# Performance work log

Hardware: AMD Instinct MI355X
Metric: run time of the kernel (lower is better)

Reference implementation:

```python
import jax, jax.numpy as jnp
import numpy as np

B, SEQ, D, H, L, DFF, K = 2, 2048, 256, 8, 2, 1024, 3
DK = D // H
EPS = 1e-5
DROP_CONNECT = 0.5  # eval mode: weight * (1 - rate)


def _make_pe():
    pos = np.arange(SEQ)[:, None].astype(np.float32)
    div = np.exp(np.arange(0, D, 2).astype(np.float32) * (-np.log(10000.0) / D))
    pe = np.zeros((SEQ, D), np.float32)
    pe[:, 0::2] = np.sin(pos * div)
    pe[:, 1::2] = np.cos(pos * div)
    return jnp.asarray(pe)


def setup_inputs() -> dict:
    key = jax.random.key(0)
    ks = jax.random.split(key, 16)
    s = 0.02
    d = {
        'x': jax.random.normal(ks[0], (B, SEQ, 1), jnp.float32),
        'conv_w': jax.random.normal(ks[1], (D, 1, K), jnp.float32) * s,
        'conv_b': jnp.zeros((D,), jnp.float32),
        'bn_g': jnp.ones((D,), jnp.float32),
        'bn_b': jnp.zeros((D,), jnp.float32),
        'pe': _make_pe(),
        'qW': jax.random.normal(ks[2], (L, D, D), jnp.float32) * s,
        'qb': jnp.zeros((L, D), jnp.float32),
        'kW': jax.random.normal(ks[3], (L, D, D), jnp.float32) * s,
        'kb': jnp.zeros((L, D), jnp.float32),
        'vW': jax.random.normal(ks[4], (L, D, D), jnp.float32) * s,
        'vb': jnp.zeros((L, D), jnp.float32),
        'oW': jax.random.normal(ks[5], (L, D, D), jnp.float32) * s,
        'ob': jnp.zeros((L, D), jnp.float32),
        'scale': jnp.ones((L,), jnp.float32),
        'td': jnp.ones((L, H), jnp.float32),
        'ln1g': jnp.ones((L, D), jnp.float32),
        'ln1b': jnp.zeros((L, D), jnp.float32),
        'f1W': jax.random.normal(ks[6], (L, DFF, D), jnp.float32) * s,
        'f1b': jnp.zeros((L, DFF), jnp.float32),
        'f2W': jax.random.normal(ks[7], (L, D, DFF), jnp.float32) * s,
        'f2b': jnp.zeros((L, D), jnp.float32),
        'ln2g': jnp.ones((L, D), jnp.float32),
        'ln2b': jnp.zeros((L, D), jnp.float32),
        'outW': jax.random.normal(ks[8], (1, D), jnp.float32) * s,
        'outb': jnp.zeros((1,), jnp.float32),
    }
    return d


def _layernorm(z, g, b):
    m = z.mean(-1, keepdims=True)
    v = ((z - m) ** 2).mean(-1, keepdims=True)
    return (z - m) / jnp.sqrt(v + EPS) * g + b


def reference(x, conv_w, conv_b, bn_g, bn_b, pe, qW, qb, kW, kb, vW, vb, oW, ob,
              scale, td, ln1g, ln1b, f1W, f1b, f2W, f2b, ln2g, ln2b, outW, outb):
    # CNN frontend: [B,S,1] -> [B,1,S] -> conv -> BN(eval) -> relu -> [B,S,D]
    h = jnp.transpose(x, (0, 2, 1))
    h = jax.lax.conv_general_dilated(h, conv_w, (1,), 'SAME',
                                     dimension_numbers=('NCH', 'OIH', 'NCH'))
    h = h + conv_b[None, :, None]
    # BatchNorm eval with running_mean=0, running_var=1
    h = h / jnp.sqrt(1.0 + EPS) * bn_g[None, :, None] + bn_b[None, :, None]
    h = jax.nn.relu(h)
    h = jnp.transpose(h, (0, 2, 1)) + pe[None]

    inv_sqrt_dk = 1.0 / np.sqrt(DK).astype(np.float32)
    key_pos = jnp.arange(SEQ, dtype=h.dtype)  # decay depends on key index only

    for l in range(L):
        q = (h @ qW[l].T + qb[l]).reshape(B, SEQ, H, DK).transpose(0, 2, 1, 3)
        k = (h @ kW[l].T + kb[l]).reshape(B, SEQ, H, DK).transpose(0, 2, 1, 3)
        v = (h @ vW[l].T + vb[l]).reshape(B, SEQ, H, DK).transpose(0, 2, 1, 3)
        scores = jnp.einsum('bhqd,bhkd->bhqk', q, k) * (inv_sqrt_dk * scale[l])
        decay = jnp.exp(-td[l][:, None, None] * key_pos[None, None, :])  # [H,1,S]
        scores = scores * decay[None]
        attn = jax.nn.softmax(scores, axis=-1) * jax.nn.sigmoid(scores)
        ctx = jnp.einsum('bhqk,bhkd->bhqd', attn, v)
        ctx = ctx.transpose(0, 2, 1, 3).reshape(B, SEQ, D)
        h = _layernorm(h + (ctx @ oW[l].T + ob[l]), ln1g[l], ln1b[l])
        ff = jax.nn.relu(h @ f1W[l].T + f1b[l]) @ f2W[l].T + f2b[l]
        h = _layernorm(h + ff, ln2g[l], ln2b[l])

    last = h[:, -1, :]
    # DropConnectLinear in eval: weight * (1 - drop_connect_rate)
    return last @ (outW * (1.0 - DROP_CONNECT)).T + outb
```

## Files before the change

### kernel.cpp

```cpp
#include <hip/hip_runtime.h>
#include <math.h>

#define B_    2
#define SEQ_  2048
#define D_    256
#define H_    8
#define DK_   32
#define L_    2
#define DFF_  1024

#define TD_CUT 44.0f

typedef short  bf16x8 __attribute__((ext_vector_type(8)));
typedef float  f32x4  __attribute__((ext_vector_type(4)));

__device__ __forceinline__ int compute_kcut(float tdv) {
    int kcut = SEQ_;
    if (tdv > 1e-9f) {
        float kc = TD_CUT / tdv;
        kcut = (kc >= (float)SEQ_) ? SEQ_ : ((int)kc + 1);
    }
    int kcr = (kcut + 63) & ~63;
    if (kcr > SEQ_) kcr = SEQ_;
    return kcr;
}

__device__ __forceinline__ unsigned short f2bf(float f) {
    unsigned int u = __float_as_uint(f);
    unsigned int r = u + 0x7FFFu + ((u >> 16) & 1u);
    return (unsigned short)(r >> 16);
}
__device__ __forceinline__ float bf2f(unsigned short u) {
    return __uint_as_float(((unsigned int)u) << 16);
}
__device__ __forceinline__ float bflo(unsigned int u) {
    return __uint_as_float(u << 16);
}
__device__ __forceinline__ float bfhi(unsigned int u) {
    return __uint_as_float(u & 0xFFFF0000u);
}

__device__ __forceinline__ void gload_lds16(const unsigned short* g, unsigned short* l) {
    __builtin_amdgcn_global_load_lds(
        (const __attribute__((address_space(1))) unsigned int*)(const unsigned int*)g,
        (__attribute__((address_space(3))) unsigned int*)(unsigned int*)l,
        16, 0, 0);
}

__global__ __launch_bounds__(256) void prep_kernel(
    const float* __restrict__ x, const float* __restrict__ w,
    const float* __restrict__ cb, const float* __restrict__ bg,
    const float* __restrict__ bb, const float* __restrict__ pe,
    float* __restrict__ h, unsigned short* __restrict__ hbf,
    const float* __restrict__ p0, const float* __restrict__ p1,
    const float* __restrict__ p2, const float* __restrict__ p3,
    const float* __restrict__ p4, const float* __restrict__ p5,
    unsigned short* __restrict__ q0, unsigned short* __restrict__ q1,
    unsigned short* __restrict__ q2, unsigned short* __restrict__ q3,
    unsigned short* __restrict__ q4, unsigned short* __restrict__ q5,
    float* __restrict__ hts0, float* __restrict__ hts1)
{
    int bid = blockIdx.x;
// ... 36 lines not shown

    int s0 = tile * 32;
    float xm1 = (s0 > 0) ? xp[s0 - 1] : 0.f;
    float x0v = xp[s0];
    float hsum = 0.f;
#pragma unroll 4
    for (int r = 0; r < 32; ++r) {
        int s = s0 + r;
        float xp1 = (s < SEQ_ - 1) ? xp[s + 1] : 0.f;
        float acc = xm1 * w0 + x0v * w1v + xp1 * w2v + cbd;
        acc = acc * gg + bbd;
        acc = fmaxf(acc, 0.f);
        float v = acc + pe[s * D_ + d];
        size_t idx = ((size_t)(b * SEQ_ + s)) * D_ + d;
        h[idx] = v;
        unsigned short ub = f2bf(v);
        hbf[idx] = ub;
        hsum += bf2f(ub);
        xm1 = x0v; x0v = xp1;
    }
    hts0[(b * 64 + tile) * 256 + d] = hsum;
}

__global__ __launch_bounds__(256) void gemm_qkv(
    const unsigned short* __restrict__ A,
    const unsigned short* __restrict__ W0, const unsigned short* __restrict__ W1,
    const unsigned short* __restrict__ W2,
    const float* __restrict__ b0, const float* __restrict__ b1,
    const float* __restrict__ b2,
    unsigned short* __restrict__ O0, unsigned short* __restrict__ O1,
    unsigned short* __restrict__ O2,
    const float* __restrict__ td_l,
    const float* __restrict__ hts_l, float* __restrict__ vts_g,
    int M, int N, int K)
{
    __shared__ unsigned short As[2][2][2048];
    __shared__ unsigned short Bs[2][2][2048];
    __shared__ float hsc[256];

    int z = blockIdx.z;
    int tid  = threadIdx.x;

    if (z == 3) {
        if (blockIdx.x != 0 || blockIdx.y >= 16) return;
        int hh = blockIdx.y & 7;
        int b  = blockIdx.y >> 3;
        int kcr = compute_kcut(td_l[hh]);
        if (kcr >= SEQ_) return;
        int tcut = kcr >> 5;
        const float* hb = hts_l + (size_t)b * 64 * 256 + tid;
        float s = 0.f;
#pragma unroll
        for (int t = 0; t < 64; ++t) {
            float v = hb[t * 256];
            s += (t >= tcut) ? v : 0.f;
        }
        hsc[tid] = s;
        __syncthreads();
        int j = tid >> 3, e = tid & 7;
        const unsigned short* wrow = W2 + (size_t)(hh * 32 + j) * 256 + e * 32;
        float dot = 0.f;
#pragma unroll
        for (int i = 0; i < 4; ++i) {
            bf16x8 w8 = *(const bf16x8*)(wrow + i * 8);
#pragma unroll
            for (int t2 = 0; t2 < 8; ++t2)
                dot += hsc[e * 32 + i * 8 + t2] * bf2f((unsigned short)w8[t2]);
        }
        dot += __shfl_xor(dot, 1);
        dot += __shfl_xor(dot, 2);
        dot += __shfl_xor(dot, 4);
        if (e == 0)
            vts_g[(b * H_ + hh) * 32 + j] = dot + (float)(SEQ_ - kcr) * b2[hh * 32 + j];
        return;
    }

    int bm = blockIdx.y * 64, bn = blockIdx.x * 64;
    if (z > 0) {
        float tdmin = td_l[0];
#pragma unroll
        for (int i = 1; i < H_; ++i) tdmin = fminf(tdmin, td_l[i]);
        if ((bm & (SEQ_ - 1)) >= compute_kcut(tdmin)) return;
    }
    const unsigned short* W = (z == 0) ? W0 : (z == 1) ? W1 : W2;
    const float* bias = (z == 0) ? b0 : (z == 1) ? b1 : b2;
    unsigned short* C = (z == 0) ? O0 : (z == 1) ? O1 : O2;

    int wave = tid >> 6, lane = tid & 63;
    int wm = (wave & 1) * 32, wn = (wave >> 1) * 32;

    int sr  = tid >> 2;
    int scb = (tid & 3) ^ ((sr >> 1) & 3);
    const unsigned short* aG = A + (size_t)(bm + sr) * K + scb * 8;
    const unsigned short* wG = W + (size_t)(bn + sr) * K + scb * 8;

    int fr = lane & 15;
    int kb = lane >> 4;
    int cbo = (kb ^ ((fr >> 1) & 3)) * 8;
    int oA0 = (wm + fr) * 32 + cbo;
    int oA1 = (wm + 16 + fr) * 32 + cbo;
    int oB0 = (wn + fr) * 32 + cbo;
    int oB1 = (wn + 16 + fr) * 32 + cbo;

    f32x4 acc[2][2];
#pragma unroll
    for (int i = 0; i < 2; ++i)
#pragma unroll
        for (int j = 0; j < 2; ++j) acc[i][j] = (f32x4){0.f, 0.f, 0.f, 0.f};

    auto stage = [&](int s, int dd) {
        gload_lds16(aG + s * 64,      &As[dd][0][tid * 8]);
        gload_lds16(aG + s * 64 + 32, &As[dd][1][tid * 8]);
        gload_lds16(wG + s * 64,      &Bs[dd][0][tid * 8]);
        gload_lds16(wG + s * 64 + 32, &Bs[dd][1][tid * 8]);
    };

    int nst = K >> 6;
    stage(0, 0);
    __syncthreads();
    for (int s = 0; s < nst; ++s) {
        int dd = s & 1;
        if (s + 1 < nst) stage(s + 1, dd ^ 1);
#pragma unroll
        for (int kk = 0; kk < 2; ++kk) {
            bf16x8 a0f = *(const bf16x8*)&As[dd][kk][oA0];
            bf16x8 a1f = *(const bf16x8*)&As[dd][kk][oA1];
            bf16x8 b0f = *(const bf16x8*)&Bs[dd][kk][oB0];
            bf16x8 b1f = *(const bf16x8*)&Bs[dd][kk][oB1];
            acc[0][0] = __builtin_amdgcn_mfma_f32_16x16x32_bf16(a0f, b0f, acc[0][0], 0, 0, 0);
            acc[0][1] = __builtin_amdgcn_mfma_f32_16x16x32_bf16(a0f, b1f, acc[0][1], 0, 0, 0);
            acc[1][0] = __builtin_amdgcn_mfma_f32_16x16x32_bf16(a1f, b0f, acc[1][0], 0, 0, 0);
            acc[1][1] = __builtin_amdgcn_mfma_f32_16x16x32_bf16(a1f, b1f, acc[1][1], 0, 0, 0);
        }
        __syncthreads();
    }

    int crow = (lane >> 4) * 4;
    int ccol = lane & 15;
#pragma unroll
    for (int j = 0; j < 2; ++j) {
        float bj = bias[bn + wn + j * 16 + ccol];
#pragma unroll
        for (int i = 0; i < 2; ++i) {
#pragma unroll
            for (int r = 0; r < 4; ++r) {
                float v = acc[i][j][r] + bj;
                C[(size_t)(bm + wm + i * 16 + crow + r) * N + bn + wn + j * 16 + ccol] = f2bf(v);
            }
        }
    }
}

__global__ __launch_bounds__(256) void attn_kernel(
    const unsigned short* __restrict__ q, const unsigned short* __restrict__ k,
    const unsigned short* __restrict__ v, const float* __restrict__ vts_g,
    unsigned short* __restrict__ ctxbf,
    const float* __restrict__ scale_p, const float* __restrict__ td_l)
{
    int b = blockIdx.z, hh = blockIdx.y;
    int tid = threadIdx.x;
    int wave = tid >> 6, lane = tid & 63;
    int q0r = blockIdx.x * 64;

    float sc  = 0.17677669529663687f * scale_p[0];
    float tdv = td_l[hh];
    int kcr = compute_kcut(tdv);
    int ntiles = kcr >> 6;

    __shared__ unsigned short qt[64 * 32];
    __shared__ unsigned short kt[64 * 32];
    __shared__ unsigned short vtT[32 * 72];
    __shared__ unsigned short pl[64 * 72];
    __shared__ float vts_s[32];

    if (tid < 32) vts_s[tid] = vts_g[(b * H_ + hh) * 32 + tid];

    int srow = tid >> 2, sseg = tid & 3;
    gload_lds16(q + ((size_t)(b * SEQ_ + q0r + srow)) * D_ + hh * DK_ + sseg * 8,
                &qt[tid * 8]);

    int fr = lane & 15, kb = lane >> 4;
    const unsigned short* qfrag = &qt[(wave * 16 + fr) * 32 + kb * 8];

    f32x4 acc_o[2];
    acc_o[0] = (f32x4){0.f, 0.f, 0.f, 0.f};
    acc_o[1] = (f32x4){0.f, 0.f, 0.f, 0.f};
    float lpart[4] = {0.f, 0.f, 0.f, 0.f};

    for (int t = 0; t < ntiles; ++t) {
        int k0 = t * 64;
        if (t > 0) __syncthreads();
        {
            gload_lds16(k + ((size_t)(b * SEQ_ + k0 + srow)) * D_ + hh * DK_ + sseg * 8,
                        &kt[tid * 8]);
            const unsigned short* vp =
                v + ((size_t)(b * SEQ_ + k0 + srow)) * D_ + hh * DK_ + sseg * 8;
            uint4 uv = *(const uint4*)vp;
            unsigned short ve[8];
            ve[0] = (unsigned short)(uv.x); ve[1] = (unsigned short)(uv.x >> 16);
            ve[2] = (unsigned short)(uv.y); ve[3] = (unsigned short)(uv.y >> 16);
            ve[4] = (unsigned short)(uv.z); ve[5] = (unsigned short)(uv.z >> 16);
            ve[6] = (unsigned short)(uv.w); ve[7] = (unsigned short)(uv.w >> 16);
#pragma unroll
            for (int e = 0; e < 8; ++e)
                vtT[(sseg * 8 + e) * 72 + srow] = ve[e];
        }
        __syncthreads();

        f32x4 acc_s[4];
        bf16x8 aq = *(const bf16x8*)qfrag;
#pragma unroll
        for (int kt_i = 0; kt_i < 4; ++kt_i) {
            bf16x8 bk = *(const bf16x8*)&kt[(kt_i * 16 + fr) * 32 + kb * 8];
            acc_s[kt_i] = __builtin_amdgcn_mfma_f32_16x16x32_bf16(
                aq, bk, (f32x4){0.f, 0.f, 0.f, 0.f}, 0, 0, 0);
        }
#pragma unroll
        for (int kt_i = 0; kt_i < 4; ++kt_i) {
#pragma unroll
            for (int r = 0; r < 4; ++r) {
                int key = k0 + kt_i * 16 + fr;
                float sv = acc_s[kt_i][r] * sc * __expf(-tdv * (float)key);
                float e  = __expf(sv);
                float sg = 1.f / (1.f + __expf(-sv));
                lpart[r] += e;
                int qrow = wave * 16 + kb * 4 + r;
                pl[qrow * 72 + kt_i * 16 + fr] = f2bf(e * sg);
            }
        }
        __syncthreads();

#pragma unroll
        for (int ks = 0; ks < 2; ++ks) {
            bf16x8 pa = *(const bf16x8*)&pl[(wave * 16 + fr) * 72 + ks * 32 + kb * 8];
#pragma unroll
            for (int nt = 0; nt < 2; ++nt) {
                bf16x8 vb8 = *(const bf16x8*)&vtT[(nt * 16 + fr) * 72 + ks * 32 + kb * 8];
                acc_o[nt] = __builtin_amdgcn_mfma_f32_16x16x32_bf16(pa, vb8, acc_o[nt], 0, 0, 0);
            }
        }
    }

#pragma unroll
    for (int r = 0; r < 4; ++r) {
        lpart[r] += __shfl_xor(lpart[r], 1);
        lpart[r] += __shfl_xor(lpart[r], 2);
        lpart[r] += __shfl_xor(lpart[r], 4);
        lpart[r] += __shfl_xor(lpart[r], 8);
    }
    float taill = (kcr < SEQ_) ? (float)(SEQ_ - kcr) : 0.f;

#pragma unroll
    for (int nt = 0; nt < 2; ++nt) {
        float vadd = (kcr < SEQ_) ? 0.5f * vts_s[nt * 16 + fr] : 0.f;
#pragma unroll
        for (int r = 0; r < 4; ++r) {
            float invL = 1.f / (lpart[r] + taill);
            float o = (acc_o[nt][r] + vadd) * invL;
            int qrow = q0r + wave * 16 + kb * 4 + r;
            ctxbf[((size_t)(b * SEQ_ + qrow)) * D_ + hh * DK_ + nt * 16 + fr] = f2bf(o);
        }
    }
}

__global__ __launch_bounds__(256) void oproj_ln1(
    const unsigned short* __restrict__ ctx, const unsigned short* __restrict__ wo,
    const float* __restrict__ ob, const float* __restrict__ resid,
    const float* __restrict__ g1, const float* __restrict__ bt1,
    float* __restrict__ h1out, unsigned short* __restrict__ h1bf)
{
    __shared__ unsigned short As[2][512];
    __shared__ unsigned short Bs[2][8192];
    __shared__ float lsum[4][16], lsq[4][16], mean_s[16], inv_s[16];

    int tid = threadIdx.x;
    int wave = tid >> 6, lane = tid & 63;
    int bm = blockIdx.x * 16;
    int fr = lane & 15, kb = lane >> 4;
    int q = kb, cl = fr;
    int swz = (fr >> 1) & 3;

    const unsigned short* gpB[4];
    int dstB[4];
// ... 77 lines not shown
        float sq = lsq[0][tid] + lsq[1][tid] + lsq[2][tid] + lsq[3][tid];
        float mean = s * (1.f / 256.f);
        float var  = sq * (1.f / 256.f) - mean * mean;
        mean_s[tid] = mean;
        inv_s[tid]  = rsqrtf(var + 1e-5f);
    }
    __syncthreads();

#pragma unroll
    for (int ct = 0; ct < 4; ++ct) {
        int col = wave * 64 + ct * 16 + cl;
        float gc = g1[col], bc = bt1[col];
#pragma unroll
        for (int r = 0; r < 4; ++r) {
            int lr = q * 4 + r;
            float o = (zv[ct][r] - mean_s[lr]) * inv_s[lr] * gc + bc;
            size_t off = (size_t)(bm + lr) * 256 + col;
            h1out[off] = o;
            h1bf[off]  = f2bf(o);
        }
    }
}

__global__ __launch_bounds__(256) void ffn_fused(
    const unsigned short* __restrict__ h1bf, const unsigned short* __restrict__ w1,
    const float* __restrict__ f1b, const unsigned short* __restrict__ w2,
    float* __restrict__ part)
{
    __shared__ unsigned short As[2][1024];
    __shared__ unsigned short Bs[2][8192];
    __shared__ unsigned short ffs[32 * 264];

    int tid = threadIdx.x;
    int wave = tid >> 6, lane = tid & 63;
    int c = blockIdx.x;
    int bm = blockIdx.y * 32;
    int fr = lane & 15, kb = lane >> 4;
    int q = kb, cl = fr;

    const unsigned short* gB1[4];
    const unsigned short* gB2[4];
    int dstB[4];
#pragma unroll
    for (int i = 0; i < 4; ++i) {
        int sB = i * 256 + tid;
        int r = sB >> 2, ck = (sB & 3) ^ ((r >> 1) & 3);
        gB1[i] = w1 + (size_t)(c * 256 + r) * 256 + ck * 8;
        gB2[i] = w2 + (size_t)r * 1024 + c * 256 + ck * 8;
        dstB[i] = sB * 8;
    }
    const unsigned short* gA = nullptr;
    if (tid < 128) {
        int ar = tid >> 2, ack = (tid & 3) ^ ((ar >> 1) & 3);
        gA = h1bf + (size_t)(bm + ar) * 256 + ack * 8;
    }

    int oA1[2], oB[4];
#pragma unroll
    for (int t = 0; t < 2; ++t) {
        int m = t * 16 + fr;
        oA1[t] = m * 32 + ((kb ^ ((m >> 1) & 3)) * 8);
    }
#pragma unroll
    for (int t = 0; t < 4; ++t) {
        int n = wave * 64 + t * 16 + fr;
        oB[t] = n * 32 + ((kb ^ ((n >> 1) & 3)) * 8);
    }

    auto stage1 = [&](int s, int dd) {
#pragma unroll
        for (int i = 0; i < 4; ++i) gload_lds16(gB1[i] + s * 32, &Bs[dd][dstB[i]]);
        if (tid < 128) gload_lds16(gA + s * 32, &As[dd][tid * 8]);
    };
    auto stage2 = [&](int s, int dd) {
#pragma unroll
        for (int i = 0; i < 4; ++i) gload_lds16(gB2[i] + s * 32, &Bs[dd][dstB[i]]);
    };

    f32x4 a1[2][4];
#pragma unroll
    for (int i = 0; i < 2; ++i)
#pragma unroll
        for (int j = 0; j < 4; ++j) a1[i][j] = (f32x4){0.f, 0.f, 0.f, 0.f};

    stage1(0, 0);
    __syncthreads();
    for (int ks = 0; ks < 8; ++ks) {
        int dd = ks & 1;
        if (ks + 1 < 8) stage1(ks + 1, dd ^ 1);
        bf16x8 af[2], bfv[4];
#pragma unroll
        for (int t = 0; t < 2; ++t) af[t] = *(const bf16x8*)&As[dd][oA1[t]];
#pragma unroll
        for (int t = 0; t < 4; ++t) bfv[t] = *(const bf16x8*)&Bs[dd][oB[t]];
#pragma unroll
        for (int i = 0; i < 2; ++i)
#pragma unroll
            for (int j = 0; j < 4; ++j)
                a1[i][j] = __builtin_amdgcn_mfma_f32_16x16x32_bf16(af[i], bfv[j], a1[i][j], 0, 0, 0);
        __syncthreads();
    }

#pragma unroll
    for (int ct = 0; ct < 4; ++ct) {
        int col = wave * 64 + ct * 16 + cl;
        float bj = f1b[c * 256 + col];
#pragma unroll
        for (int rt = 0; rt < 2; ++rt)
#pragma unroll
            for (int r = 0; r < 4; ++r) {
                float v = fmaxf(a1[rt][ct][r] + bj, 0.f);
                ffs[(rt * 16 + q * 4 + r) * 264 + col] = f2bf(v);
            }
    }

    f32x4 a2[2][4];
#pragma unroll
    for (int i = 0; i < 2; ++i)
#pragma unroll
        for (int j = 0; j < 4; ++j) a2[i][j] = (f32x4){0.f, 0.f, 0.f, 0.f};

    stage2(0, 0);
    __syncthreads();
    for (int ks = 0; ks < 8; ++ks) {
        int dd = ks & 1;
        if (ks + 1 < 8) stage2(ks + 1, dd ^ 1);
        bf16x8 af[2], bfv[4];
#pragma unroll
        for (int t = 0; t < 2; ++t)
            af[t] = *(const bf16x8*)&ffs[(t * 16 + fr) * 264 + ks * 32 + kb * 8];
#pragma unroll
        for (int t = 0; t < 4; ++t) bfv[t] = *(const bf16x8*)&Bs[dd][oB[t]];
#pragma unroll
        for (int i = 0; i < 2; ++i)
#pragma unroll
            for (int j = 0; j < 4; ++j)
                a2[i][j] = __builtin_amdgcn_mfma_f32_16x16x32_bf16(af[i], bfv[j], a2[i][j], 0, 0, 0);
        __syncthreads();
    }

#pragma unroll
    for (int ct = 0; ct < 4; ++ct) {
        int col = wave * 64 + ct * 16 + cl;
#pragma unroll
        for (int rt = 0; rt < 2; ++rt)
#pragma unroll
            for (int r = 0; r < 4; ++r)
                part[((size_t)c * 4096 + bm + rt * 16 + q * 4 + r) * 256 + col] = a2[rt][ct][r];
    }
}

__global__ __launch_bounds__(256) void merge_ln2(
    const float* __restrict__ h1, const float* __restrict__ part,
    const float* __restrict__ f2b, const float* __restrict__ g2,
    const float* __restrict__ bt2,
    float* __restrict__ hout, unsigned short* __restrict__ hbf,
    const float* __restrict__ outW, const float* __restrict__ outb,
    float* __restrict__ out, int doFinal,
    float* __restrict__ hts1, int doHts)
{
    __shared__ float red[4][256];

    int wrp = threadIdx.x >> 6;
    int row = blockIdx.x * 4 + wrp;
    int lane = threadIdx.x & 63;
    int d = lane * 4;

    float4 z = *(const float4*)(h1 + (size_t)row * 256 + d);
    float4 b4 = *(const float4*)(f2b + d);
    z.x += b4.x; z.y += b4.y; z.z += b4.z; z.w += b4.w;
#pragma unroll
    for (int c = 0; c < 4; ++c) {
        float4 p = *(const float4*)(part + ((size_t)c * 4096 + row) * 256 + d);
        z.x += p.x; z.y += p.y; z.z += p.z; z.w += p.w;
    }

    float s = z.x + z.y + z.z + z.w;
    float ss = z.x * z.x + z.y * z.y + z.z * z.z + z.w * z.w;
#pragma unroll
    for (int off = 1; off < 64; off <<= 1) {
        s += __shfl_xor(s, off);
        ss += __shfl_xor(ss, off);
    }
    float mean = s * (1.f / 256.f);
    float var = ss * (1.f / 256.f) - mean * mean;
    float inv = rsqrtf(var + 1e-5f);

    float4 g4 = *(const float4*)(g2 + d);
    float4 t4 = *(const float4*)(bt2 + d);
    float4 o;
    o.x = (z.x - mean) * inv * g4.x + t4.x;
    o.y = (z.y - mean) * inv * g4.y + t4.y;
    o.z = (z.z - mean) * inv * g4.z + t4.z;
    o.w = (z.w - mean) * inv * g4.w + t4.w;
    *(float4*)(hout + (size_t)row * 256 + d) = o;
    unsigned short s0 = f2bf(o.x), s1 = f2bf(o.y), s2 = f2bf(o.z), s3 = f2bf(o.w);
    unsigned int u01 = (unsigned)s0 | ((unsigned)s1 << 16);
    unsigned int u23 = (unsigned)s2 | ((unsigned)s3 << 16);
    *(uint2*)&hbf[(size_t)row * 256 + d] = make_uint2(u01, u23);

    if (doHts) {
        *(float4*)&red[wrp][d] = make_float4(bf2f(s0), bf2f(s1), bf2f(s2), bf2f(s3));
        __syncthreads();
        int cidx = threadIdx.x;
        float cs = red[0][cidx] + red[1][cidx] + red[2][cidx] + red[3][cidx];
        int b = blockIdx.x >> 9;
        int tile = (blockIdx.x >> 3) & 63;
        atomicAdd(&hts1[((b << 6) + tile) * 256 + cidx], cs);
    }

    if (doFinal && (row == 2047 || row == 4095)) {
        float4 w4 = *(const float4*)(outW + d);
        float s2f = o.x * w4.x + o.y * w4.y + o.z * w4.z + o.w * w4.w;
#pragma unroll
        for (int off = 1; off < 64; off <<= 1) s2f += __shfl_xor(s2f, off);
        if (lane == 0) out[row >> 11] = s2f * 0.5f + outb[0];
    }
}

extern "C" void kernel_launch(void* const* d_in, const int* in_sizes, int n_in,
                              void* d_out, int out_size, void* d_ws, size_t ws_size,
                              hipStream_t stream)
{
    (void)in_sizes; (void)n_in; (void)out_size; (void)ws_size;
    const float* x      = (const float*)d_in[0];
    const float* conv_w = (const float*)d_in[1];
    const float* conv_b = (const float*)d_in[2];
    const float* bn_g   = (const float*)d_in[3];
    const float* bn_b   = (const float*)d_in[4];
    const float* pe     = (const float*)d_in[5];
    const float* qW     = (const float*)d_in[6];
    const float* qb     = (const float*)d_in[7];
    const float* kW     = (const float*)d_in[8];
    const float* kb     = (const float*)d_in[9];
    const float* vW     = (const float*)d_in[10];
    const float* vb     = (const float*)d_in[11];
    const float* oW     = (const float*)d_in[12];
    const float* ob     = (const float*)d_in[13];
    const float* scale  = (const float*)d_in[14];
// ... 2 lines not shown
    const float* ln1b   = (const float*)d_in[17];
    const float* f1W    = (const float*)d_in[18];
    const float* f1b    = (const float*)d_in[19];
    const float* f2W    = (const float*)d_in[20];
    const float* f2b    = (const float*)d_in[21];
    const float* ln2g   = (const float*)d_in[22];
    const float* ln2b   = (const float*)d_in[23];
    const float* outW   = (const float*)d_in[24];
    const float* outb   = (const float*)d_in[25];
    float* out = (float*)d_out;

    float* ws = (float*)d_ws;
    const size_t MT = (size_t)B_ * SEQ_ * D_;
    const size_t HTS = (size_t)B_ * 64 * 256;
    float* h     = ws;
    float* h1    = ws + MT;
    float* part  = ws + 2 * MT;
    float* hts0  = ws + 6 * MT;
    float* hts1  = hts0 + HTS;
    float* vts_g = hts1 + HTS;
    unsigned short* bfb = (unsigned short*)(vts_g + 512);
    unsigned short* h_bf   = bfb;
    unsigned short* ctx_bf = bfb + MT;
    unsigned short* q_bf   = bfb + 2 * MT;
    unsigned short* k_bf   = bfb + 3 * MT;
    unsigned short* v_bf   = bfb + 4 * MT;
    unsigned short* h1_bf  = bfb + 5 * MT;
    unsigned short* wq_bf  = bfb + 6 * MT;
    unsigned short* wk_bf  = wq_bf + MT / 8;
    unsigned short* wv_bf  = wk_bf + MT / 8;
    unsigned short* wo_bf  = wv_bf + MT / 8;
    unsigned short* wf1_bf = wo_bf + MT / 8;
    unsigned short* wf2_bf = wf1_bf + MT / 2;

    const int Mrows = B_ * SEQ_;

    prep_kernel<<<768 + 128, 256, 0, stream>>>(
        x, conv_w, conv_b, bn_g, bn_b, pe, h, h_bf,
        qW, kW, vW, oW, f1W, f2W,
        wq_bf, wk_bf, wv_bf, wo_bf, wf1_bf, wf2_bf, hts0, hts1);

    for (int l = 0; l < L_; ++l) {
        const unsigned short* wq_l  = wq_bf  + (size_t)l * D_ * D_;
        const unsigned short* wk_l  = wk_bf  + (size_t)l * D_ * D_;
        const unsigned short* wv_l  = wv_bf  + (size_t)l * D_ * D_;
        const unsigned short* wo_l  = wo_bf  + (size_t)l * D_ * D_;
        const unsigned short* wf1_l = wf1_bf + (size_t)l * DFF_ * D_;
        const unsigned short* wf2_l = wf2_bf + (size_t)l * DFF_ * D_;
        const float* hts_l = (l == 0) ? hts0 : hts1;

        gemm_qkv<<<dim3(D_ / 64, Mrows / 64, 4), 256, 0, stream>>>(
            h_bf, wq_l, wk_l, wv_l, qb + l * D_, kb + l * D_, vb + l * D_,
            q_bf, k_bf, v_bf, td + l * H_, hts_l, vts_g, Mrows, D_, D_);

        attn_kernel<<<dim3(SEQ_ / 64, H_, B_), 256, 0, stream>>>(
            q_bf, k_bf, v_bf, vts_g, ctx_bf, scale + l, td + l * H_);

        oproj_ln1<<<Mrows / 16, 256, 0, stream>>>(
            ctx_bf, wo_l, ob + l * D_, h,
            ln1g + l * D_, ln1b + l * D_, h1, h1_bf);

        ffn_fused<<<dim3(4, Mrows / 32), 256, 0, stream>>>(
            h1_bf, wf1_l, f1b + l * DFF_, wf2_l, part);

        merge_ln2<<<Mrows / 4, 256, 0, stream>>>(
            h1, part, f2b + l * D_, ln2g + l * D_, ln2b + l * D_,
            h, h_bf, outW, outb, out, (l == L_ - 1) ? 1 : 0,
            hts1, (l == 0) ? 1 : 0);
    }
}
```

Before: 185.5 us.

## Fuse QKV projection into attention and FFN with LayerNorm2

The standalone QKV GEMM is removed, and Q/K/V projections are now computed inside the attention kernel per key tile, along with the decayed V tail sum. The FFN kernel now runs both FFN GEMMs over the full DFF per 16-row block and applies the residual plus LayerNorm2 itself, so the partial-sum buffer and merge kernel are gone. This cuts launches and the global round trips for q/k/v and the FFN partials. In exchange, each attention block recomputes K and V projections for every key tile it visits, and the FFN grid becomes smaller with a long serial loop per block.

```diff
diff --git a/kernel.cpp b/kernel.cpp
--- a/kernel.cpp
+++ b/kernel.cpp
@@ -32,12 +32,6 @@
 }
 __device__ __forceinline__ float bf2f(unsigned short u) {
     return __uint_as_float(((unsigned int)u) << 16);
-}
-__device__ __forceinline__ float bflo(unsigned int u) {
-    return __uint_as_float(u << 16);
-}
-__device__ __forceinline__ float bfhi(unsigned int u) {
-    return __uint_as_float(u & 0xFFFF0000u);
 }
 
 __device__ __forceinline__ void gload_lds16(const unsigned short* g, unsigned short* l) {
@@ -120,138 +114,13 @@
     hts0[(b * 64 + tile) * 256 + d] = hsum;
 }
 
-__global__ __launch_bounds__(256) void gemm_qkv(
-    const unsigned short* __restrict__ A,
-    const unsigned short* __restrict__ W0, const unsigned short* __restrict__ W1,
-    const unsigned short* __restrict__ W2,
-    const float* __restrict__ b0, const float* __restrict__ b1,
-    const float* __restrict__ b2,
-    unsigned short* __restrict__ O0, unsigned short* __restrict__ O1,
-    unsigned short* __restrict__ O2,
-    const float* __restrict__ td_l,
-    const float* __restrict__ hts_l, float* __restrict__ vts_g,
-    int M, int N, int K)
-{
-    __shared__ unsigned short As[2][2][2048];
-    __shared__ unsigned short Bs[2][2][2048];
-    __shared__ float hsc[256];
-
-    int z = blockIdx.z;
-    int tid  = threadIdx.x;
-
-    if (z == 3) {
-        if (blockIdx.x != 0 || blockIdx.y >= 16) return;
-        int hh = blockIdx.y & 7;
-        int b  = blockIdx.y >> 3;
-        int kcr = compute_kcut(td_l[hh]);
-        if (kcr >= SEQ_) return;
-        int tcut = kcr >> 5;
-        const float* hb = hts_l + (size_t)b * 64 * 256 + tid;
-        float s = 0.f;
-#pragma unroll
-        for (int t = 0; t < 64; ++t) {
-            float v = hb[t * 256];
-            s += (t >= tcut) ? v : 0.f;
-        }
-        hsc[tid] = s;
-        __syncthreads();
-        int j = tid >> 3, e = tid & 7;
-        const unsigned short* wrow = W2 + (size_t)(hh * 32 + j) * 256 + e * 32;
-        float dot = 0.f;
-#pragma unroll
-        for (int i = 0; i < 4; ++i) {
-            bf16x8 w8 = *(const bf16x8*)(wrow + i * 8);
-#pragma unroll
-            for (int t2 = 0; t2 < 8; ++t2)
-                dot += hsc[e * 32 + i * 8 + t2] * bf2f((unsigned short)w8[t2]);
-        }
-        dot += __shfl_xor(dot, 1);
-        dot += __shfl_xor(dot, 2);
-        dot += __shfl_xor(dot, 4);
-        if (e == 0)
-            vts_g[(b * H_ + hh) * 32 + j] = dot + (float)(SEQ_ - kcr) * b2[hh * 32 + j];
-        return;
-    }
-
-    int bm = blockIdx.y * 64, bn = blockIdx.x * 64;
-    if (z > 0) {
-        float tdmin = td_l[0];
-#pragma unroll
-        for (int i = 1; i < H_; ++i) tdmin = fminf(tdmin, td_l[i]);
-        if ((bm & (SEQ_ - 1)) >= compute_kcut(tdmin)) return;
-    }
-    const unsigned short* W = (z == 0) ? W0 : (z == 1) ? W1 : W2;
-    const float* bias = (z == 0) ? b0 : (z == 1) ? b1 : b2;
-    unsigned short* C = (z == 0) ? O0 : (z == 1) ? O1 : O2;
-
-    int wave = tid >> 6, lane = tid & 63;
-    int wm = (wave & 1) * 32, wn = (wave >> 1) * 32;
-
-    int sr  = tid >> 2;
-    int scb = (tid & 3) ^ ((sr >> 1) & 3);
-    const unsigned short* aG = A + (size_t)(bm + sr) * K + scb * 8;
-    const unsigned short* wG = W + (size_t)(bn + sr) * K + scb * 8;
-
-    int fr = lane & 15;
-    int kb = lane >> 4;
-    int cbo = (kb ^ ((fr >> 1) & 3)) * 8;
-    int oA0 = (wm + fr) * 32 + cbo;
-    int oA1 = (wm + 16 + fr) * 32 + cbo;
-    int oB0 = (wn + fr) * 32 + cbo;
-    int oB1 = (wn + 16 + fr) * 32 + cbo;
-
-    f32x4 acc[2][2];
-#pragma unroll
-    for (int i = 0; i < 2; ++i)
-#pragma unroll
-        for (int j = 0; j < 2; ++j) acc[i][j] = (f32x4){0.f, 0.f, 0.f, 0.f};
-
-    auto stage = [&](int s, int dd) {
-        gload_lds16(aG + s * 64,      &As[dd][0][tid * 8]);
-        gload_lds16(aG + s * 64 + 32, &As[dd][1][tid * 8]);
-        gload_lds16(wG + s * 64,      &Bs[dd][0][tid * 8]);
-        gload_lds16(wG + s * 64 + 32, &Bs[dd][1][tid * 8]);
-    };
-
-    int nst = K >> 6;
-    stage(0, 0);
-    __syncthreads();
-    for (int s = 0; s < nst; ++s) {
-        int dd = s & 1;
-        if (s + 1 < nst) stage(s + 1, dd ^ 1);
-#pragma unroll
-        for (int kk = 0; kk < 2; ++kk) {
-            bf16x8 a0f = *(const bf16x8*)&As[dd][kk][oA0];
-            bf16x8 a1f = *(const bf16x8*)&As[dd][kk][oA1];
-            bf16x8 b0f = *(const bf16x8*)&Bs[dd][kk][oB0];
-            bf16x8 b1f = *(const bf16x8*)&Bs[dd][kk][oB1];
-            acc[0][0] = __builtin_amdgcn_mfma_f32_16x16x32_bf16(a0f, b0f, acc[0][0], 0, 0, 0);
-            acc[0][1] = __builtin_amdgcn_mfma_f32_16x16x32_bf16(a0f, b1f, acc[0][1], 0, 0, 0);
-            acc[1][0] = __builtin_amdgcn_mfma_f32_16x16x32_bf16(a1f, b0f, acc[1][0], 0, 0, 0);
-            acc[1][1] = __builtin_amdgcn_mfma_f32_16x16x32_bf16(a1f, b1f, acc[1][1], 0, 0, 0);
-        }
-        __syncthreads();
-    }
-
-    int crow = (lane >> 4) * 4;
-    int ccol = lane & 15;
-#pragma unroll
-    for (int j = 0; j < 2; ++j) {
-        float bj = bias[bn + wn + j * 16 + ccol];
-#pragma unroll
-        for (int i = 0; i < 2; ++i) {
-#pragma unroll
-            for (int r = 0; r < 4; ++r) {
-                float v = acc[i][j][r] + bj;
-                C[(size_t)(bm + wm + i * 16 + crow + r) * N + bn + wn + j * 16 + ccol] = f2bf(v);
-            }
-        }
-    }
-}
-
-__global__ __launch_bounds__(256) void attn_kernel(
-    const unsigned short* __restrict__ q, const unsigned short* __restrict__ k,
-    const unsigned short* __restrict__ v, const float* __restrict__ vts_g,
+__global__ __launch_bounds__(256) void attn_fused(
+    const unsigned short* __restrict__ hbf,
+    const unsigned short* __restrict__ wq, const unsigned short* __restrict__ wk,
+    const unsigned short* __restrict__ wv,
+    const float* __restrict__ qbp, const float* __restrict__ kbp,
+    const float* __restrict__ vbp,
+    const float* __restrict__ hts_l,
     unsigned short* __restrict__ ctxbf,
     const float* __restrict__ scale_p, const float* __restrict__ td_l)
 {
@@ -259,59 +128,134 @@
     int tid = threadIdx.x;
     int wave = tid >> 6, lane = tid & 63;
     int q0r = blockIdx.x * 64;
+    size_t bq = (size_t)b * SEQ_;
 
     float sc  = 0.17677669529663687f * scale_p[0];
     float tdv = td_l[hh];
     int kcr = compute_kcut(tdv);
     int ntiles = kcr >> 6;
 
-    __shared__ unsigned short qt[64 * 32];
-    __shared__ unsigned short kt[64 * 32];
+    __shared__ unsigned short hq_s[2048];
+    __shared__ unsigned short hk_s[2048];
+    __shared__ unsigned short wq_s[1024];
+    __shared__ unsigned short wk_s[1024];
+    __shared__ unsigned short wv_s[1024];
+    __shared__ unsigned short qt[64 * 40];
+    __shared__ unsigned short kt[64 * 40];
     __shared__ unsigned short vtT[32 * 72];
     __shared__ unsigned short pl[64 * 72];
+    __shared__ float hsc[256];
     __shared__ float vts_s[32];
 
-    if (tid < 32) vts_s[tid] = vts_g[(b * H_ + hh) * 32 + tid];
-
-    int srow = tid >> 2, sseg = tid & 3;
-    gload_lds16(q + ((size_t)(b * SEQ_ + q0r + srow)) * D_ + hh * DK_ + sseg * 8,
-                &qt[tid * 8]);
-
+    if (kcr < SEQ_) {
+        int tcut = kcr >> 5;
+        const float* hb = hts_l + (size_t)b * 64 * 256 + tid;
+        float s = 0.f;
+#pragma unroll
+        for (int t = 0; t < 64; ++t) {
+            float v = hb[t * 256];
+            s += (t >= tcut) ? v : 0.f;
+        }
+        hsc[tid] = s;
+        __syncthreads();
+        int j = tid >> 3, e = tid & 7;
+        const bf16x8* wp = (const bf16x8*)(wv + (size_t)(hh * 32 + j) * 256 + e * 32);
+        float dot = 0.f;
+#pragma unroll
+        for (int i = 0; i < 4; ++i) {
+            bf16x8 w8 = wp[i];
+#pragma unroll
+            for (int t2 = 0; t2 < 8; ++t2)
+                dot += hsc[e * 32 + i * 8 + t2] * bf2f((unsigned short)w8[t2]);
+        }
+        dot += __shfl_xor(dot, 1);
+        dot += __shfl_xor(dot, 2);
+        dot += __shfl_xor(dot, 4);
+        if (e == 0) vts_s[j] = dot + (float)(SEQ_ - kcr) * vbp[hh * 32 + j];
+    }
+
+    int sr = tid >> 2, scb = (tid & 3) ^ ((sr >> 1) & 3);
+    int wtid = tid & 127, wr = wtid >> 2;
+    int wck = (wtid & 3) ^ ((wr >> 1) & 3);
     int fr = lane & 15, kb = lane >> 4;
-    const unsigned short* qfrag = &qt[(wave * 16 + fr) * 32 + kb * 8];
-
-    f32x4 acc_o[2];
-    acc_o[0] = (f32x4){0.f, 0.f, 0.f, 0.f};
-    acc_o[1] = (f32x4){0.f, 0.f, 0.f, 0.f};
+    int cbo = (kb ^ ((fr >> 1) & 3)) * 8;
+    int ccol = fr, crow = kb * 4;
+
+    f32x4 acc_q[2], acc_o[2];
+    acc_q[0] = acc_q[1] = (f32x4){0.f, 0.f, 0.f, 0.f};
+    acc_o[0] = acc_o[1] = (f32x4){0.f, 0.f, 0.f, 0.f};
     float lpart[4] = {0.f, 0.f, 0.f, 0.f};
 
     for (int t = 0; t < ntiles; ++t) {
         int k0 = t * 64;
-        if (t > 0) __syncthreads();
-        {
-            gload_lds16(k + ((size_t)(b * SEQ_ + k0 + srow)) * D_ + hh * DK_ + sseg * 8,
-                        &kt[tid * 8]);
-            const unsigned short* vp =
-                v + ((size_t)(b * SEQ_ + k0 + srow)) * D_ + hh * DK_ + sseg * 8;
-            uint4 uv = *(const uint4*)vp;
-            unsigned short ve[8];
-            ve[0] = (unsigned short)(uv.x); ve[1] = (unsigned short)(uv.x >> 16);
-            ve[2] = (unsigned short)(uv.y); ve[3] = (unsigned short)(uv.y >> 16);
-            ve[4] = (unsigned short)(uv.z); ve[5] = (unsigned short)(uv.z >> 16);
-            ve[6] = (unsigned short)(uv.w); ve[7] = (unsigned short)(uv.w >> 16);
-#pragma unroll
-            for (int e = 0; e < 8; ++e)
-                vtT[(sseg * 8 + e) * 72 + srow] = ve[e];
+        f32x4 acc_k[2], acc_v[2];
+        acc_k[0] = acc_k[1] = (f32x4){0.f, 0.f, 0.f, 0.f};
+        acc_v[0] = acc_v[1] = (f32x4){0.f, 0.f, 0.f, 0.f};
+
+        for (int ks = 0; ks < 8; ++ks) {
+            __syncthreads();
+            if (t == 0)
+                gload_lds16(hbf + (bq + q0r + sr) * 256 + ks * 32 + scb * 8, &hq_s[tid * 8]);
+            gload_lds16(hbf + (bq + k0 + sr) * 256 + ks * 32 + scb * 8, &hk_s[tid * 8]);
+            if (tid < 128) {
+                gload_lds16(wq + (size_t)(hh * 32 + wr) * 256 + ks * 32 + wck * 8, &wq_s[wtid * 8]);
+                gload_lds16(wv + (size_t)(hh * 32 + wr) * 256 + ks * 32 + wck * 8, &wv_s[wtid * 8]);
+            } else {
+                gload_lds16(wk + (size_t)(hh * 32 + wr) * 256 + ks * 32 + wck * 8, &wk_s[wtid * 8]);
+            }
+            __syncthreads();
+
+            bf16x8 ak  = *(const bf16x8*)&hk_s[(wave * 16 + fr) * 32 + cbo];
+            bf16x8 bk0 = *(const bf16x8*)&wk_s[fr * 32 + cbo];
+            bf16x8 bk1 = *(const bf16x8*)&wk_s[(16 + fr) * 32 + cbo];
+            bf16x8 av0 = *(const bf16x8*)&wv_s[fr * 32 + cbo];
+            bf16x8 av1 = *(const bf16x8*)&wv_s[(16 + fr) * 32 + cbo];
+            acc_k[0] = __builtin_amdgcn_mfma_f32_16x16x32_bf16(ak, bk0, acc_k[0], 0, 0, 0);
+            acc_k[1] = __builtin_amdgcn_mfma_f32_16x16x32_bf16(ak, bk1, acc_k[1], 0, 0, 0);
+            acc_v[0] = __builtin_amdgcn_mfma_f32_16x16x32_bf16(av0, ak, acc_v[0], 0, 0, 0);
+            acc_v[1] = __builtin_amdgcn_mfma_f32_16x16x32_bf16(av1, ak, acc_v[1], 0, 0, 0);
+            if (t == 0) {
+                bf16x8 aq  = *(const bf16x8*)&hq_s[(wave * 16 + fr) * 32 + cbo];
+                bf16x8 bq0 = *(const bf16x8*)&wq_s[fr * 32 + cbo];
+                bf16x8 bq1 = *(const bf16x8*)&wq_s[(16 + fr) * 32 + cbo];
+                acc_q[0] = __builtin_amdgcn_mfma_f32_16x16x32_bf16(aq, bq0, acc_q[0], 0, 0, 0);
+                acc_q[1] = __builtin_amdgcn_mfma_f32_16x16x32_bf16(aq, bq1, acc_q[1], 0, 0, 0);
+            }
+        }
+
+        if (t == 0) {
+#pragma unroll
+            for (int n = 0; n < 2; ++n) {
+                float bj = qbp[hh * 32 + n * 16 + ccol];
+#pragma unroll
+                for (int r = 0; r < 4; ++r)
+                    qt[(wave * 16 + crow + r) * 40 + n * 16 + ccol] = f2bf(acc_q[n][r] + bj);
+            }
+        }
+#pragma unroll
+        for (int n = 0; n < 2; ++n) {
+            float bj = kbp[hh * 32 + n * 16 + ccol];
+#pragma unroll
+            for (int r = 0; r < 4; ++r)
+                kt[(wave * 16 + crow + r) * 40 + n * 16 + ccol] = f2bf(acc_k[n][r] + bj);
+        }
+#pragma unroll
+        for (int d = 0; d < 2; ++d) {
+#pragma unroll
+            for (int r = 0; r < 4; ++r) {
+                int dim = d * 16 + crow + r;
+                vtT[dim * 72 + wave * 16 + ccol] = f2bf(acc_v[d][r] + vbp[hh * 32 + dim]);
+            }
         }
         __syncthreads();
 
+        bf16x8 aq8 = *(const bf16x8*)&qt[(wave * 16 + fr) * 40 + kb * 8];
         f32x4 acc_s[4];
-        bf16x8 aq = *(const bf16x8*)qfrag;
 #pragma unroll
         for (int kt_i = 0; kt_i < 4; ++kt_i) {
-            bf16x8 bk = *(const bf16x8*)&kt[(kt_i * 16 + fr) * 32 + kb * 8];
+            bf16x8 bk8 = *(const bf16x8*)&kt[(kt_i * 16 + fr) * 40 + kb * 8];
             acc_s[kt_i] = __builtin_amdgcn_mfma_f32_16x16x32_bf16(
-                aq, bk, (f32x4){0.f, 0.f, 0.f, 0.f}, 0, 0, 0);
+                aq8, bk8, (f32x4){0.f, 0.f, 0.f, 0.f}, 0, 0, 0);
         }
 #pragma unroll
         for (int kt_i = 0; kt_i < 4; ++kt_i) {
@@ -322,18 +266,17 @@
                 float e  = __expf(sv);
                 float sg = 1.f / (1.f + __expf(-sv));
                 lpart[r] += e;
-                int qrow = wave * 16 + kb * 4 + r;
-                pl[qrow * 72 + kt_i * 16 + fr] = f2bf(e * sg);
+                pl[(wave * 16 + crow + r) * 72 + kt_i * 16 + fr] = f2bf(e * sg);
             }
         }
         __syncthreads();
 
 #pragma unroll
-        for (int ks = 0; ks < 2; ++ks) {
-            bf16x8 pa = *(const bf16x8*)&pl[(wave * 16 + fr) * 72 + ks * 32 + kb * 8];
+        for (int ks2 = 0; ks2 < 2; ++ks2) {
+            bf16x8 pa = *(const bf16x8*)&pl[(wave * 16 + fr) * 72 + ks2 * 32 + kb * 8];
 #pragma unroll
             for (int nt = 0; nt < 2; ++nt) {
-                bf16x8 vb8 = *(const bf16x8*)&vtT[(nt * 16 + fr) * 72 + ks * 32 + kb * 8];
+                bf16x8 vb8 = *(const bf16x8*)&vtT[(nt * 16 + fr) * 72 + ks2 * 32 + kb * 8];
                 acc_o[nt] = __builtin_amdgcn_mfma_f32_16x16x32_bf16(pa, vb8, acc_o[nt], 0, 0, 0);
             }
         }
@@ -355,8 +298,8 @@
         for (int r = 0; r < 4; ++r) {
             float invL = 1.f / (lpart[r] + taill);
             float o = (acc_o[nt][r] + vadd) * invL;
-            int qrow = q0r + wave * 16 + kb * 4 + r;
-            ctxbf[((size_t)(b * SEQ_ + qrow)) * D_ + hh * DK_ + nt * 16 + fr] = f2bf(o);
+            int qrow = q0r + wave * 16 + crow + r;
+            ctxbf[(bq + qrow) * D_ + hh * DK_ + nt * 16 + fr] = f2bf(o);
         }
     }
 }
@@ -480,199 +423,191 @@
     }
 }
 
-__global__ __launch_bounds__(256) void ffn_fused(
+__global__ __launch_bounds__(256) void ffn_ln2(
     const unsigned short* __restrict__ h1bf, const unsigned short* __restrict__ w1,
     const float* __restrict__ f1b, const unsigned short* __restrict__ w2,
-    float* __restrict__ part)
-{
-    __shared__ unsigned short As[2][1024];
-    __shared__ unsigned short Bs[2][8192];
-    __shared__ unsigned short ffs[32 * 264];
-
-    int tid = threadIdx.x;
-    int wave = tid >> 6, lane = tid & 63;
-    int c = blockIdx.x;
-    int bm = blockIdx.y * 32;
-    int fr = lane & 15, kb = lane >> 4;
-    int q = kb, cl = fr;
-
-    const unsigned short* gB1[4];
-    const unsigned short* gB2[4];
-    int dstB[4];
-#pragma unroll
-    for (int i = 0; i < 4; ++i) {
-        int sB = i * 256 + tid;
-        int r = sB >> 2, ck = (sB & 3) ^ ((r >> 1) & 3);
-        gB1[i] = w1 + (size_t)(c * 256 + r) * 256 + ck * 8;
-        gB2[i] = w2 + (size_t)r * 1024 + c * 256 + ck * 8;
-        dstB[i] = sB * 8;
-    }
-    const unsigned short* gA = nullptr;
-    if (tid < 128) {
-        int ar = tid >> 2, ack = (tid & 3) ^ ((ar >> 1) & 3);
-        gA = h1bf + (size_t)(bm + ar) * 256 + ack * 8;
-    }
-
-    int oA1[2], oB[4];
-#pragma unroll
-    for (int t = 0; t < 2; ++t) {
-        int m = t * 16 + fr;
-        oA1[t] = m * 32 + ((kb ^ ((m >> 1) & 3)) * 8);
-    }
-#pragma unroll
-    for (int t = 0; t < 4; ++t) {
-        int n = wave * 64 + t * 16 + fr;
-        oB[t] = n * 32 + ((kb ^ ((n >> 1) & 3)) * 8);
-    }
-
-    auto stage1 = [&](int s, int dd) {
-#pragma unroll
-        for (int i = 0; i < 4; ++i) gload_lds16(gB1[i] + s * 32, &Bs[dd][dstB[i]]);
-        if (tid < 128) gload_lds16(gA + s * 32, &As[dd][tid * 8]);
-    };
-    auto stage2 = [&](int s, int dd) {
-#pragma unroll
-        for (int i = 0; i < 4; ++i) gload_lds16(gB2[i] + s * 32, &Bs[dd][dstB[i]]);
-    };
-
-    f32x4 a1[2][4];
-#pragma unroll
-    for (int i = 0; i < 2; ++i)
-#pragma unroll
-        for (int j = 0; j < 4; ++j) a1[i][j] = (f32x4){0.f, 0.f, 0.f, 0.f};
-
-    stage1(0, 0);
-    __syncthreads();
-    for (int ks = 0; ks < 8; ++ks) {
-        int dd = ks & 1;
-        if (ks + 1 < 8) stage1(ks + 1, dd ^ 1);
-        bf16x8 af[2], bfv[4];
-#pragma unroll
-        for (int t = 0; t < 2; ++t) af[t] = *(const bf16x8*)&As[dd][oA1[t]];
-#pragma unroll
-        for (int t = 0; t < 4; ++t) bfv[t] = *(const bf16x8*)&Bs[dd][oB[t]];
-#pragma unroll
-        for (int i = 0; i < 2; ++i)
-#pragma unroll
-            for (int j = 0; j < 4; ++j)
-                a1[i][j] = __builtin_amdgcn_mfma_f32_16x16x32_bf16(af[i], bfv[j], a1[i][j], 0, 0, 0);
-        __syncthreads();
-    }
-
-#pragma unroll
-    for (int ct = 0; ct < 4; ++ct) {
-        int col = wave * 64 + ct * 16 + cl;
-        float bj = f1b[c * 256 + col];
-#pragma unroll
-        for (int rt = 0; rt < 2; ++rt)
-#pragma unroll
-            for (int r = 0; r < 4; ++r) {
-                float v = fmaxf(a1[rt][ct][r] + bj, 0.f);
-                ffs[(rt * 16 + q * 4 + r) * 264 + col] = f2bf(v);
-            }
-    }
-
-    f32x4 a2[2][4];
-#pragma unroll
-    for (int i = 0; i < 2; ++i)
-#pragma unroll
-        for (int j = 0; j < 4; ++j) a2[i][j] = (f32x4){0.f, 0.f, 0.f, 0.f};
-
-    stage2(0, 0);
-    __syncthreads();
-    for (int ks = 0; ks < 8; ++ks) {
-        int dd = ks & 1;
-        if (ks + 1 < 8) stage2(ks + 1, dd ^ 1);
-        bf16x8 af[2], bfv[4];
-#pragma unroll
-        for (int t = 0; t < 2; ++t)
-            af[t] = *(const bf16x8*)&ffs[(t * 16 + fr) * 264 + ks * 32 + kb * 8];
-#pragma unroll
-        for (int t = 0; t < 4; ++t) bfv[t] = *(const bf16x8*)&Bs[dd][oB[t]];
-#pragma unroll
-        for (int i = 0; i < 2; ++i)
-#pragma unroll
-            for (int j = 0; j < 4; ++j)
-                a2[i][j] = __builtin_amdgcn_mfma_f32_16x16x32_bf16(af[i], bfv[j], a2[i][j], 0, 0, 0);
-        __syncthreads();
-    }
-
-#pragma unroll
-    for (int ct = 0; ct < 4; ++ct) {
-        int col = wave * 64 + ct * 16 + cl;
-#pragma unroll
-        for (int rt = 0; rt < 2; ++rt)
-#pragma unroll
-            for (int r = 0; r < 4; ++r)
-                part[((size_t)c * 4096 + bm + rt * 16 + q * 4 + r) * 256 + col] = a2[rt][ct][r];
-    }
-}
-
-__global__ __launch_bounds__(256) void merge_ln2(
-    const float* __restrict__ h1, const float* __restrict__ part,
-    const float* __restrict__ f2b, const float* __restrict__ g2,
-    const float* __restrict__ bt2,
+    const float* __restrict__ h1, const float* __restrict__ f2b,
+    const float* __restrict__ g2, const float* __restrict__ bt2,
     float* __restrict__ hout, unsigned short* __restrict__ hbf,
     const float* __restrict__ outW, const float* __restrict__ outb,
     float* __restrict__ out, int doFinal,
     float* __restrict__ hts1, int doHts)
 {
-    __shared__ float red[4][256];
-
-    int wrp = threadIdx.x >> 6;
-    int row = blockIdx.x * 4 + wrp;
-    int lane = threadIdx.x & 63;
-    int d = lane * 4;
-
-    float4 z = *(const float4*)(h1 + (size_t)row * 256 + d);
-    float4 b4 = *(const float4*)(f2b + d);
-    z.x += b4.x; z.y += b4.y; z.z += b4.z; z.w += b4.w;
-#pragma unroll
-    for (int c = 0; c < 4; ++c) {
-        float4 p = *(const float4*)(part + ((size_t)c * 4096 + row) * 256 + d);
-        z.x += p.x; z.y += p.y; z.z += p.z; z.w += p.w;
-    }
-
-    float s = z.x + z.y + z.z + z.w;
-    float ss = z.x * z.x + z.y * z.y + z.z * z.z + z.w * z.w;
-#pragma unroll
-    for (int off = 1; off < 64; off <<= 1) {
-        s += __shfl_xor(s, off);
-        ss += __shfl_xor(ss, off);
-    }
-    float mean = s * (1.f / 256.f);
-    float var = ss * (1.f / 256.f) - mean * mean;
-    float inv = rsqrtf(var + 1e-5f);
-
-    float4 g4 = *(const float4*)(g2 + d);
-    float4 t4 = *(const float4*)(bt2 + d);
-    float4 o;
-    o.x = (z.x - mean) * inv * g4.x + t4.x;
-    o.y = (z.y - mean) * inv * g4.y + t4.y;
-    o.z = (z.z - mean) * inv * g4.z + t4.z;
-    o.w = (z.w - mean) * inv * g4.w + t4.w;
-    *(float4*)(hout + (size_t)row * 256 + d) = o;
-    unsigned short s0 = f2bf(o.x), s1 = f2bf(o.y), s2 = f2bf(o.z), s3 = f2bf(o.w);
-    unsigned int u01 = (unsigned)s0 | ((unsigned)s1 << 16);
-    unsigned int u23 = (unsigned)s2 | ((unsigned)s3 << 16);
-    *(uint2*)&hbf[(size_t)row * 256 + d] = make_uint2(u01, u23);
+    __shared__ unsigned short As[8 * 512];
+    __shared__ unsigned short Bs[2][8192];
+    __shared__ unsigned short ffs[16 * 264];
+    __shared__ float lsum[4][16], lsq[4][16], mean_s[16], inv_s[16];
+    __shared__ float red2[64];
+
+    int tid = threadIdx.x;
+    int wave = tid >> 6, lane = tid & 63;
+    int bm = blockIdx.x * 16;
+    int fr = lane & 15, kb = lane >> 4;
+    int q = kb, cl = fr;
+
+    int oA_s = fr * 32 + ((kb ^ ((fr >> 1) & 3)) * 8);
+    int oB[4];
+#pragma unroll
+    for (int t = 0; t < 4; ++t) {
+        int n = wave * 64 + t * 16 + fr;
+        oB[t] = n * 32 + ((kb ^ ((fr >> 1) & 3)) * 8);
+    }
+
+    auto stageW = [&](int u, int dd) {
+        int c = u >> 4, ph = (u >> 3) & 1, ks = u & 7;
+#pragma unroll
+        for (int i = 0; i < 4; ++i) {
+            int sB = i * 256 + tid;
+            int r = sB >> 2, ck = (sB & 3) ^ ((r >> 1) & 3);
+            const unsigned short* src = (ph == 0)
+                ? w1 + (size_t)(c * 256 + r) * 256 + ks * 32 + ck * 8
+                : w2 + (size_t)r * 1024 + c * 256 + ks * 32 + ck * 8;
+            gload_lds16(src, &Bs[dd][sB * 8]);
+        }
+    };
+
+#pragma unroll
+    for (int rd = 0; rd < 2; ++rd) {
+        int s = rd * 256 + tid;
+        int ksl = s >> 6, wseg = s & 63, r = wseg >> 2, j = wseg & 3;
+        int ck = j ^ ((r >> 1) & 3);
+        gload_lds16(h1bf + (size_t)(bm + r) * 256 + ksl * 32 + ck * 8, &As[s * 8]);
+    }
+    stageW(0, 0);
+    __syncthreads();
+
+    f32x4 acc2[4], a1[4];
+#pragma unroll
+    for (int j = 0; j < 4; ++j) acc2[j] = (f32x4){0.f, 0.f, 0.f, 0.f};
+
+    for (int u = 0; u < 64; ++u) {
+        int dd = u & 1;
+        int ph = (u >> 3) & 1, ks = u & 7, c = u >> 4;
+        if (u + 1 < 64) stageW(u + 1, dd ^ 1);
+        if ((u & 15) == 0) {
+#pragma unroll
+            for (int j = 0; j < 4; ++j) a1[j] = (f32x4){0.f, 0.f, 0.f, 0.f};
+        }
+        if ((u & 15) == 8) {
+#pragma unroll
+            for (int ct = 0; ct < 4; ++ct) {
+                int col = wave * 64 + ct * 16 + cl;
+                float bj = f1b[c * 256 + col];
+#pragma unroll
+                for (int r = 0; r < 4; ++r) {
+                    float v = fmaxf(a1[ct][r] + bj, 0.f);
+                    ffs[(q * 4 + r) * 264 + col] = f2bf(v);
+                }
+            }
+            __syncthreads();
+        }
+        bf16x8 bfv[4];
+#pragma unroll
+        for (int t2 = 0; t2 < 4; ++t2) bfv[t2] = *(const bf16x8*)&Bs[dd][oB[t2]];
+        if (ph == 0) {
+            bf16x8 af = *(const bf16x8*)&As[ks * 512 + oA_s];
+#pragma unroll
+            for (int j = 0; j < 4; ++j)
+                a1[j] = __builtin_amdgcn_mfma_f32_16x16x32_bf16(af, bfv[j], a1[j], 0, 0, 0);
+        } else {
+            bf16x8 af = *(const bf16x8*)&ffs[fr * 264 + ks * 32 + kb * 8];
+#pragma unroll
+            for (int j = 0; j < 4; ++j)
+                acc2[j] = __builtin_amdgcn_mfma_f32_16x16x32_bf16(af, bfv[j], acc2[j], 0, 0, 0);
+        }
+        __syncthreads();
+    }
+
+    float zsum[4] = {0.f, 0.f, 0.f, 0.f}, zsq[4] = {0.f, 0.f, 0.f, 0.f};
+    float zv[4][4];
+#pragma unroll
+    for (int ct = 0; ct < 4; ++ct) {
+        int col = wave * 64 + ct * 16 + cl;
+        float bj = f2b[col];
+#pragma unroll
+        for (int r = 0; r < 4; ++r) {
+            int row = bm + q * 4 + r;
+            float z = acc2[ct][r] + bj + h1[(size_t)row * 256 + col];
+            zv[ct][r] = z;
+            zsum[r] += z;
+            zsq[r]  += z * z;
+        }
+    }
+#pragma unroll
+    for (int r = 0; r < 4; ++r) {
+#pragma unroll
+        for (int off = 1; off < 16; off <<= 1) {
+            zsum[r] += __shfl_xor(zsum[r], off);
+            zsq[r]  += __shfl_xor(zsq[r], off);
+        }
+    }
+    if (cl == 0) {
+#pragma unroll
+        for (int r = 0; r < 4; ++r) {
+            lsum[wave][q * 4 + r] = zsum[r];
+            lsq[wave][q * 4 + r]  = zsq[r];
+        }
+    }
+    __syncthreads();
+    if (tid < 16) {
+        float s  = lsum[0][tid] + lsum[1][tid] + lsum[2][tid] + lsum[3][tid];
+        float sq = lsq[0][tid] + lsq[1][tid] + lsq[2][tid] + lsq[3][tid];
+        float mean = s * (1.f / 256.f);
+        float var  = sq * (1.f / 256.f) - mean * mean;
+        mean_s[tid] = mean;
+        inv_s[tid]  = rsqrtf(var + 1e-5f);
+    }
+    __syncthreads();
+
+    float hsum[4] = {0.f, 0.f, 0.f, 0.f};
+#pragma unroll
+    for (int ct = 0; ct < 4; ++ct) {
+        int col = wave * 64 + ct * 16 + cl;
+        float gc = g2[col], bc = bt2[col];
+#pragma unroll
+        for (int r = 0; r < 4; ++r) {
+            int lr = q * 4 + r;
+            float o = (zv[ct][r] - mean_s[lr]) * inv_s[lr] * gc + bc;
+            size_t off = (size_t)(bm + lr) * 256 + col;
+            hout[off] = o;
+            unsigned short ub = f2bf(o);
+            hbf[off] = ub;
+            hsum[ct] += bf2f(ub);
+        }
+    }
 
     if (doHts) {
-        *(float4*)&red[wrp][d] = make_float4(bf2f(s0), bf2f(s1), bf2f(s2), bf2f(s3));
+#pragma unroll
+        for (int ct = 0; ct < 4; ++ct) {
+            hsum[ct] += __shfl_xor(hsum[ct], 16);
+            hsum[ct] += __shfl_xor(hsum[ct], 32);
+        }
+        if (kb == 0) {
+            int bb = blockIdx.x >> 7;
+            int tile = (blockIdx.x & 127) >> 1;
+#pragma unroll
+            for (int ct = 0; ct < 4; ++ct)
+                atomicAdd(&hts1[((bb << 6) + tile) * 256 + wave * 64 + ct * 16 + cl], hsum[ct]);
+        }
+    }
+
+    if (doFinal && (blockIdx.x == 127 || blockIdx.x == 255)) {
+        if (kb == 3) {
+            float part = 0.f;
+#pragma unroll
+            for (int ct = 0; ct < 4; ++ct) {
+                int col = wave * 64 + ct * 16 + cl;
+                float o = (zv[ct][3] - mean_s[15]) * inv_s[15] * g2[col] + bt2[col];
+                part += o * outW[col];
+            }
+            red2[wave * 16 + fr] = part;
+        }
         __syncthreads();
-        int cidx = threadIdx.x;
-        float cs = red[0][cidx] + red[1][cidx] + red[2][cidx] + red[3][cidx];
-        int b = blockIdx.x >> 9;
-        int tile = (blockIdx.x >> 3) & 63;
-        atomicAdd(&hts1[((b << 6) + tile) * 256 + cidx], cs);
-    }
-
-    if (doFinal && (row == 2047 || row == 4095)) {
-        float4 w4 = *(const float4*)(outW + d);
-        float s2f = o.x * w4.x + o.y * w4.y + o.z * w4.z + o.w * w4.w;
-#pragma unroll
-        for (int off = 1; off < 64; off <<= 1) s2f += __shfl_xor(s2f, off);
-        if (lane == 0) out[row >> 11] = s2f * 0.5f + outb[0];
+        if (tid == 0) {
+            float s2 = 0.f;
+            for (int i2 = 0; i2 < 64; ++i2) s2 += red2[i2];
+            out[blockIdx.x >> 7] = s2 * 0.5f + outb[0];
+        }
     }
 }
 
@@ -721,9 +656,6 @@
     unsigned short* bfb = (unsigned short*)(vts_g + 512);
     unsigned short* h_bf   = bfb;
     unsigned short* ctx_bf = bfb + MT;
-    unsigned short* q_bf   = bfb + 2 * MT;
-    unsigned short* k_bf   = bfb + 3 * MT;
-    unsigned short* v_bf   = bfb + 4 * MT;
     unsigned short* h1_bf  = bfb + 5 * MT;
     unsigned short* wq_bf  = bfb + 6 * MT;
     unsigned short* wk_bf  = wq_bf + MT / 8;
@@ -731,6 +663,7 @@
     unsigned short* wo_bf  = wv_bf + MT / 8;
     unsigned short* wf1_bf = wo_bf + MT / 8;
     unsigned short* wf2_bf = wf1_bf + MT / 2;
+    (void)part;
 
     const int Mrows = B_ * SEQ_;
 
@@ -748,22 +681,18 @@
         const unsigned short* wf2_l = wf2_bf + (size_t)l * DFF_ * D_;
         const float* hts_l = (l == 0) ? hts0 : hts1;
 
-        gemm_qkv<<<dim3(D_ / 64, Mrows / 64, 4), 256, 0, stream>>>(
-            h_bf, wq_l, wk_l, wv_l, qb + l * D_, kb + l * D_, vb + l * D_,
-            q_bf, k_bf, v_bf, td + l * H_, hts_l, vts_g, Mrows, D_, D_);
-
-        attn_kernel<<<dim3(SEQ_ / 64, H_, B_), 256, 0, stream>>>(
-            q_bf, k_bf, v_bf, vts_g, ctx_bf, scale + l, td + l * H_);
+        attn_fused<<<dim3(SEQ_ / 64, H_, B_), 256, 0, stream>>>(
+            h_bf, wq_l, wk_l, wv_l,
+            qb + l * D_, kb + l * D_, vb + l * D_,
+            hts_l, ctx_bf, scale + l, td + l * H_);
 
         oproj_ln1<<<Mrows / 16, 256, 0, stream>>>(
             ctx_bf, wo_l, ob + l * D_, h,
             ln1g + l * D_, ln1b + l * D_, h1, h1_bf);
 
-        ffn_fused<<<dim3(4, Mrows / 32), 256, 0, stream>>>(
-            h1_bf, wf1_l, f1b + l * DFF_, wf2_l, part);
-
-        merge_ln2<<<Mrows / 4, 256, 0, stream>>>(
-            h1, part, f2b + l * D_, ln2g + l * D_, ln2b + l * D_,
+        ffn_ln2<<<Mrows / 16, 256, 0, stream>>>(
+            h1_bf, wf1_l, f1b + l * DFF_, wf2_l,
+            h1, f2b + l * D_, ln2g + l * D_, ln2b + l * D_,
             h, h_bf, outW, outb, out, (l == L_ - 1) ? 1 : 0,
             hts1, (l == 0) ? 1 : 0);
     }
```

New measurement: 251.4 us. 1.36x slower.
